# Performance work log

Measured on AMD Instinct MI355X. Metric: run time of the kernel, lower is better.

## Reference

```python
import jax, jax.numpy as jnp
import numpy as np

N, D, H_HEADS = 2048, 1024, 16
HD = D // H_HEADS  # per-head dim = 64
LN_EPS = 1e-5


def setup_inputs() -> dict:
    key = jax.random.key(0)
    ks = jax.random.split(key, 6)
    s = 1.0 / np.sqrt(D)  # keep pre-softmax logits in a sane range
    return {
        "X": jax.random.normal(ks[0], (N, D), dtype=jnp.float32),
        "Wq": jax.random.normal(ks[1], (D, D), dtype=jnp.float32) * s,
        "bq": jnp.zeros((D,), jnp.float32),
        "Wk": jax.random.normal(ks[2], (D, D), dtype=jnp.float32) * s,
        "bk": jnp.zeros((D,), jnp.float32),
        "Wv": jax.random.normal(ks[3], (D, D), dtype=jnp.float32) * s,
        "bv": jnp.zeros((D,), jnp.float32),
        "Wo": jax.random.normal(ks[4], (D, D), dtype=jnp.float32) * s,
        "bo": jnp.zeros((D,), jnp.float32),
        "ln_g": jnp.ones((D,), jnp.float32),
        "ln_b": jnp.zeros((D,), jnp.float32),
    }


def reference(X, Wq, bq, Wk, bk, Wv, bv, Wo, bo, ln_g, ln_b):
    n = X.shape[0]
    # QKV projections -> [h, N, HD]  (matches .view(N, h, -1).transpose(0, 1))
    q = (X @ Wq + bq).reshape(n, H_HEADS, HD).swapaxes(0, 1)
    k = (X @ Wk + bk).reshape(n, H_HEADS, HD).swapaxes(0, 1)
    v = (X @ Wv + bv).reshape(n, H_HEADS, HD).swapaxes(0, 1)
    # Unscaled attention scores (original has NO 1/sqrt(d) factor): [h, N, N]
    A = jnp.einsum('hnd,hmd->hnm', q, k)
    # Diagonal self-exclusion mask
    diag = jnp.eye(n, dtype=bool)
    A = jnp.where(diag[None, :, :], -jnp.inf, A)
    p = jax.nn.softmax(A, axis=-1)
    Oh = jnp.einsum('hnm,hmd->hnd', p, v)  # [h, N, HD]
    # Faithful replication of Oh.transpose(1,2).contiguous().view(N, d):
    # [h, N, HD] -> [h, HD, N] -> reshape to [N, D]
    O = Oh.swapaxes(1, 2).reshape(n, D)
    # Out-proj (dropout is identity in eval mode) + residual + LayerNorm
    Y = X + (O @ Wo + bo)
    mu = jnp.mean(Y, axis=-1, keepdims=True)
    var = jnp.var(Y, axis=-1, keepdims=True)
    return (Y - mu) * jax.lax.rsqrt(var + LN_EPS) * ln_g + ln_b
```

## Files before the change

### kernel.cpp

```cpp
#include <hip/hip_runtime.h>
#include <math.h>


#define NTOK 2048
#define DM   1024
#define NH   16
#define HDIM 64
#define LOG2E 1.4426950408889634f

typedef __attribute__((ext_vector_type(8))) short bf16x8;
typedef __attribute__((ext_vector_type(4))) float f32x4;

#define FRL(op, ch, st, l, e) (((((op) * 2 + (ch)) * 4 + (st)) * 64 + (l)) * 8 + (e))
#define FRO(ch, st, l, e) ((((ch) * 4 + (st)) * 64 + (l)) * 8 + (e))
#define MFMA(a, b, c) __builtin_amdgcn_mfma_f32_16x16x32_bf16(a, b, c, 0, 0, 0)

__device__ __forceinline__ unsigned short f2bf(float f) {
  unsigned u = __float_as_uint(f);
  u += 0x7FFF + ((u >> 16) & 1);
  return (unsigned short)(u >> 16);
}
__device__ __forceinline__ float bf2f(unsigned short h) {
  return __uint_as_float(((unsigned)h) << 16);
}
__device__ __forceinline__ void gload16(const unsigned short* g, unsigned short* l) {
  __builtin_amdgcn_global_load_lds(
      (const __attribute__((address_space(1))) unsigned int*)g,
      (__attribute__((address_space(3))) unsigned int*)l, 16, 0, 0);
}

__global__ __launch_bounds__(256) void cvt_x_blob(
    const float* __restrict__ X, unsigned short* __restrict__ XB)
{
  __shared__ __align__(16) unsigned short img[8192];
  const int kt = blockIdx.x, rt = blockIdx.y, tid = threadIdx.x;
  #pragma unroll
  for (int s = 0; s < 4; ++s) {
    const int f = tid + s * 256;
    const int rl = f >> 4, c4 = (f & 15) * 4;
    const float4 v = *(const float4*)(X + (size_t)(rt * 64 + rl) * DM + kt * 64 + c4);
    const float vv[4] = {v.x, v.y, v.z, v.w};
    unsigned short hi[4], lo[4];
    #pragma unroll
    for (int e = 0; e < 4; ++e) {
      hi[e] = f2bf(vv[e]);
      lo[e] = f2bf(vv[e] - bf2f(hi[e]));
    }
    const int ch = c4 >> 5, c32 = c4 & 31;
    const int gp = (c32 & 15) >> 2, e0 = (c32 >> 4) * 4;
    const int l = 16 * gp + (rl & 15), sti = rl >> 4;
    *(uint2*)&img[FRL(0, ch, sti, l, e0)] =
        make_uint2(hi[0] | (hi[1] << 16), hi[2] | (hi[3] << 16));
    *(uint2*)&img[FRL(1, ch, sti, l, e0)] =
        make_uint2(lo[0] | (lo[1] << 16), lo[2] | (lo[3] << 16));
  }
  __syncthreads();
  unsigned short* out = XB + ((size_t)rt * 16 + kt) * 8192;
  #pragma unroll
  for (int s = 0; s < 4; ++s) {
    const int u = s * 256 + tid;
    *(uint4*)(out + (size_t)u * 8) = *(const uint4*)&img[(size_t)u * 8];
  }
}

__global__ __launch_bounds__(256) void cvt_w_blob(
    const float* __restrict__ W0, const float* __restrict__ W1,
    const float* __restrict__ W2, const float* __restrict__ W3,
    unsigned short* __restrict__ WB)
{
  __shared__ __align__(16) float st[64][68];
  __shared__ __align__(16) unsigned short img[8192];
  const int nt = blockIdx.x, kt = blockIdx.y, z = blockIdx.z, tid = threadIdx.x;
  const float* W = (z == 0) ? W0 : (z == 1) ? W1 : (z == 2) ? W2 : W3;
  #pragma unroll
  for (int s = 0; s < 4; ++s) {
    const int f = tid + s * 256;
    const int kl = f >> 4, n4 = (f & 15) * 4;
    const float4 v = *(const float4*)(W + (size_t)(kt * 64 + kl) * DM + nt * 64 + n4);
    *(float4*)&st[kl][n4] = v;
  }
  __syncthreads();
  #pragma unroll
  for (int s = 0; s < 4; ++s) {
    const int f = tid + s * 256;
    const int nl = f >> 4, k4 = (f & 15) * 4;
    unsigned short hi[4], lo[4];
    #pragma unroll
    for (int e = 0; e < 4; ++e) {
      const float v = st[k4 + e][nl];
      hi[e] = f2bf(v);
      lo[e] = f2bf(v - bf2f(hi[e]));
    }
    const int ch = k4 >> 5, c32 = k4 & 31;
    const int gp = (c32 & 15) >> 2, e0 = (c32 >> 4) * 4;
    const int l = 16 * gp + (nl & 15), sti = nl >> 4;
    *(uint2*)&img[FRL(0, ch, sti, l, e0)] =
        make_uint2(hi[0] | (hi[1] << 16), hi[2] | (hi[3] << 16));
    *(uint2*)&img[FRL(1, ch, sti, l, e0)] =
        make_uint2(lo[0] | (lo[1] << 16), lo[2] | (lo[3] << 16));
  }
  __syncthreads();
  unsigned short* out = WB + (size_t)z * 2097152 + ((size_t)nt * 16 + kt) * 8192;
  #pragma unroll
  for (int s = 0; s < 4; ++s) {
    const int u = s * 256 + tid;
    *(uint4*)(out + (size_t)u * 8) = *(const uint4*)&img[(size_t)u * 8];
  }
}

__global__ __launch_bounds__(256) void gemm_qkv_blob(
    const unsigned short* __restrict__ XB, const unsigned short* __restrict__ WB,
    const float* __restrict__ bq, const float* __restrict__ bk,
    const float* __restrict__ bv,
    unsigned short* __restrict__ QF, unsigned short* __restrict__ KF,
    unsigned short* __restrict__ VF)
{
  __shared__ __align__(16) unsigned short lds[32768];
  const int tid = threadIdx.x, lane = tid & 63, wid = tid >> 6;
  const int wm = wid >> 1, wn = wid & 1;
  const int bx = blockIdx.x, by = blockIdx.y, z = blockIdx.z;
  const int g = lane >> 4, c = lane & 15;

  const unsigned short* BB = WB + (size_t)z * 2097152;
  const unsigned short* bases[4] = {
      XB + ((size_t)(2 * by) * 16) * 8192, XB + ((size_t)(2 * by + 1) * 16) * 8192,
      BB + ((size_t)(2 * bx) * 16) * 8192, BB + ((size_t)(2 * bx + 1) * 16) * 8192};

  f32x4 acc[4][4];
  #pragma unroll
  for (int i = 0; i < 4; ++i)
    #pragma unroll
    for (int j = 0; j < 4; ++j) acc[i][j] = (f32x4){0.f, 0.f, 0.f, 0.f};

  for (int kt = 0; kt < 16; ++kt) {
    __syncthreads();
    #pragma unroll
    for (int s = 0; s < 16; ++s)
      gload16(bases[s >> 2] + (size_t)kt * 8192 + ((size_t)((s & 3) * 256 + tid)) * 8,
              &lds[(size_t)(s * 256 + tid) * 8]);
    __syncthreads();
    #pragma unroll
    for (int ch = 0; ch < 2; ++ch) {
      bf16x8 ah[4], al[4], bh[4], bl[4];
      #pragma unroll
      for (int f = 0; f < 4; ++f) {
        ah[f] = *(const bf16x8*)&lds[wm * 8192 + FRL(0, ch, f, lane, 0)];
        al[f] = *(const bf16x8*)&lds[wm * 8192 + FRL(1, ch, f, lane, 0)];
        bh[f] = *(const bf16x8*)&lds[16384 + wn * 8192 + FRL(0, ch, f, lane, 0)];
        bl[f] = *(const bf16x8*)&lds[16384 + wn * 8192 + FRL(1, ch, f, lane, 0)];
      }
      #pragma unroll
      for (int fm = 0; fm < 4; ++fm)
        #pragma unroll
        for (int fn = 0; fn < 4; ++fn) {
          acc[fm][fn] = MFMA(ah[fm], bh[fn], acc[fm][fn]);
          acc[fm][fn] = MFMA(ah[fm], bl[fn], acc[fm][fn]);
          acc[fm][fn] = MFMA(al[fm], bh[fn], acc[fm][fn]);
        }
    }
  }

  const float* bias = (z == 0) ? bq : (z == 1) ? bk : bv;
  unsigned short* OUTF = (z == 0) ? QF : (z == 1) ? KF : VF;

  __syncthreads();
  const int imgb = (wm * 2 + wn) * 8192;
  #pragma unroll
  for (int fm = 0; fm < 4; ++fm)
    #pragma unroll
    for (int fn = 0; fn < 4; ++fn) {
      const int col = 128 * bx + 64 * wn + 16 * fn + c;
      const float bcol = bias[col];
      #pragma unroll
      for (int r = 0; r < 4; ++r) {
        float val = acc[fm][fn][r] + bcol;
        if (z == 0) val *= LOG2E;
        const unsigned short hp = f2bf(val);
        const unsigned short lp = f2bf(val - bf2f(hp));
        int sti, l, ch_i, e;
        if (z != 2) {
          sti = fm; l = 16 * (c >> 2) + (4 * g + r);
          ch_i = fn >> 1; e = 4 * (fn & 1) + (c & 3);
        } else {
          sti = fn; l = 16 * g + c;
          ch_i = fm >> 1; e = 4 * (fm & 1) + r;
        }
        lds[imgb + FRL(0, ch_i, sti, l, e)] = hp;
        lds[imgb + FRL(1, ch_i, sti, l, e)] = lp;
      }
    }
  __syncthreads();
  #pragma unroll
  for (int s = 0; s < 16; ++s) {
    const int u = s * 256 + tid;
    const int i = s >> 2;
    const int head = 2 * bx + (i & 1), tt = 2 * by + (i >> 1);
    *(uint4*)(OUTF + ((size_t)head * 32 + tt) * 8192 + (size_t)(u & 1023) * 8) =
        *(const uint4*)&lds[(size_t)u * 8];
  }
}

__global__ __launch_bounds__(256) void gemm_out_blob(
    const unsigned short* __restrict__ OF, const unsigned short* __restrict__ WoB,
    const float* __restrict__ bo, const float* __restrict__ X,
    float* __restrict__ Y)
{
  __shared__ __align__(16) unsigned short lds[24576];
  const int tid = threadIdx.x, lane = tid & 63, wid = tid >> 6;
  const int wm = wid >> 1, wn = wid & 1;
  const int bx = blockIdx.x, by = blockIdx.y;

  const unsigned short* oa0 = OF + ((size_t)(2 * by) * 16) * 4096;
  const unsigned short* oa1 = OF + ((size_t)(2 * by + 1) * 16) * 4096;
  const unsigned short* wb0 = WoB + ((size_t)(2 * bx) * 16) * 8192;
  const unsigned short* wb1 = WoB + ((size_t)(2 * bx + 1) * 16) * 8192;

  f32x4 acc[4][4];
  #pragma unroll
  for (int i = 0; i < 4; ++i)
    #pragma unroll
    for (int j = 0; j < 4; ++j) acc[i][j] = (f32x4){0.f, 0.f, 0.f, 0.f};

  for (int kt = 0; kt < 16; ++kt) {
    __syncthreads();
    #pragma unroll
    for (int s = 0; s < 2; ++s) {
      gload16(oa0 + (size_t)kt * 4096 + (size_t)(s * 256 + tid) * 8,
              &lds[(size_t)(s * 256 + tid) * 8]);
      gload16(oa1 + (size_t)kt * 4096 + (size_t)(s * 256 + tid) * 8,
              &lds[(size_t)(512 + s * 256 + tid) * 8]);
    }
    #pragma unroll
    for (int s = 0; s < 4; ++s) {
      gload16(wb0 + (size_t)kt * 8192 + (size_t)(s * 256 + tid) * 8,
              &lds[(size_t)(1024 + s * 256 + tid) * 8]);
      gload16(wb1 + (size_t)kt * 8192 + (size_t)(s * 256 + tid) * 8,
              &lds[(size_t)(2048 + s * 256 + tid) * 8]);
    }
    __syncthreads();
    #pragma unroll
    for (int ch = 0; ch < 2; ++ch) {
      bf16x8 ah[4], bh[4], bl[4];
      #pragma unroll
      for (int f = 0; f < 4; ++f) {
        ah[f] = *(const bf16x8*)&lds[wm * 4096 + FRO(ch, f, lane, 0)];
        bh[f] = *(const bf16x8*)&lds[8192 + wn * 8192 + FRL(0, ch, f, lane, 0)];
        bl[f] = *(const bf16x8*)&lds[8192 + wn * 8192 + FRL(1, ch, f, lane, 0)];
      }
      #pragma unroll
      for (int fm = 0; fm < 4; ++fm)
        #pragma unroll
        for (int fn = 0; fn < 4; ++fn) {
          acc[fm][fn] = MFMA(ah[fm], bh[fn], acc[fm][fn]);
          acc[fm][fn] = MFMA(ah[fm], bl[fn], acc[fm][fn]);
        }
    }
  }

  const int g = lane >> 4, c = lane & 15;
  #pragma unroll
  for (int fm = 0; fm < 4; ++fm)
    #pragma unroll
    for (int fn = 0; fn < 4; ++fn) {
      const int col = 128 * bx + 64 * wn + 16 * fn + c;
      const float bcol = bo[col];
      #pragma unroll
      for (int r = 0; r < 4; ++r) {
        const int row = 128 * by + 64 * wm + 16 * fm + 4 * g + r;
        Y[(size_t)row * DM + col] =
            acc[fm][fn][r] + bcol + X[(size_t)row * DM + col];
      }
    }
}

__global__ __launch_bounds__(256) void attn_mfma3_kernel(
    const unsigned short* __restrict__ QF, const unsigned short* __restrict__ KF,
    const unsigned short* __restrict__ VF, unsigned short* __restrict__ OF)
{
  __shared__ __align__(16) unsigned short lds[32768];

  const int tid = threadIdx.x, lane = tid & 63, wv = tid >> 6;
  const int g = lane >> 4, c = lane & 15;
  const int h = blockIdx.y, tq = blockIdx.x;
  const int q0 = tq * 64;
  const int qq = q0 + 16 * wv + c;

  const unsigned short* qb = QF + ((size_t)h * 32 + tq) * 8192;
  bf16x8 qh[2], ql[2];
  #pragma unroll
  for (int ch = 0; ch < 2; ++ch) {
    qh[ch] = *(const bf16x8*)(qb + FRL(0, ch, wv, lane, 0));
    ql[ch] = *(const bf16x8*)(qb + FRL(1, ch, wv, lane, 0));
  }

  f32x4 acc_o[4];
  #pragma unroll
  for (int df = 0; df < 4; ++df) acc_o[df] = (f32x4){0.f, 0.f, 0.f, 0.f};
  float m_run = -INFINITY, l_run = 0.f;

  const size_t hbase = (size_t)h * 32;
  {
    const unsigned short* kb = KF + hbase * 8192;
    const unsigned short* vb = VF + hbase * 8192;
    #pragma unroll
    for (int s = 0; s < 4; ++s) {
      gload16(kb + (size_t)(s * 256 + tid) * 8, &lds[(size_t)(s * 256 + tid) * 8]);
      gload16(vb + (size_t)(s * 256 + tid) * 8, &lds[8192 + (size_t)(s * 256 + tid) * 8]);
    }
  }

  int buf = 0;
  for (int kt = 0; kt < NTOK / 64; ++kt) {
    __syncthreads();
    if (kt + 1 < NTOK / 64) {
      const unsigned short* kb = KF + (hbase + kt + 1) * 8192;
      const unsigned short* vb = VF + (hbase + kt + 1) * 8192;
      unsigned short* lk = &lds[(buf ^ 1) * 16384];
      #pragma unroll
      for (int s = 0; s < 4; ++s) {
        gload16(kb + (size_t)(s * 256 + tid) * 8, lk + (size_t)(s * 256 + tid) * 8);
        gload16(vb + (size_t)(s * 256 + tid) * 8, lk + 8192 + (size_t)(s * 256 + tid) * 8);
      }
    }
    const unsigned short* lk = &lds[buf * 16384];
    const unsigned short* lv = lk + 8192;

    f32x4 sacc[4];
    #pragma unroll
    for (int fm = 0; fm < 4; ++fm) sacc[fm] = (f32x4){0.f, 0.f, 0.f, 0.f};
    __builtin_amdgcn_s_setprio(1);
    #pragma unroll
    for (int ch = 0; ch < 2; ++ch) {
      #pragma unroll
      for (int fm = 0; fm < 4; ++fm) {
        const bf16x8 khf = *(const bf16x8*)&lk[FRL(0, ch, fm, lane, 0)];
        const bf16x8 klf = *(const bf16x8*)&lk[FRL(1, ch, fm, lane, 0)];
        sacc[fm] = MFMA(khf, qh[ch], sacc[fm]);
        sacc[fm] = MFMA(khf, ql[ch], sacc[fm]);
        sacc[fm] = MFMA(klf, qh[ch], sacc[fm]);
      }
    }
    __builtin_amdgcn_s_setprio(0);

    const int tok0 = kt * 64 + 4 * g;
    #pragma unroll
    for (int fm = 0; fm < 4; ++fm)
      #pragma unroll
      for (int r = 0; r < 4; ++r)
        if (tok0 + 16 * fm + r == qq) sacc[fm][r] = -INFINITY;

    float m = -INFINITY;
    #pragma unroll
    for (int fm = 0; fm < 4; ++fm)
      #pragma unroll
      for (int r = 0; r < 4; ++r) m = fmaxf(m, sacc[fm][r]);
    m = fmaxf(m, __shfl_xor(m, 16, 64));
    m = fmaxf(m, __shfl_xor(m, 32, 64));
    const float mnew = fmaxf(m_run, m);
    const float scal = exp2f(m_run - mnew);
    float ps = 0.f;
    #pragma unroll
    for (int fm = 0; fm < 4; ++fm)
      #pragma unroll
      for (int r = 0; r < 4; ++r) {
        const float p = exp2f(sacc[fm][r] - mnew);
        sacc[fm][r] = p;
        ps += p;
      }
    ps += __shfl_xor(ps, 16, 64);
    ps += __shfl_xor(ps, 32, 64);
    l_run = l_run * scal + ps;
    m_run = mnew;

    bf16x8 ph[2];
    #pragma unroll
    for (int ch = 0; ch < 2; ++ch)
      #pragma unroll
      for (int i = 0; i < 8; ++i)
        ph[ch][i] = (short)f2bf(sacc[2 * ch + (i >> 2)][i & 3]);

    #pragma unroll
    for (int df = 0; df < 4; ++df)
      #pragma unroll
      for (int r = 0; r < 4; ++r) acc_o[df][r] *= scal;
    __builtin_amdgcn_s_setprio(1);
    #pragma unroll
    for (int ch = 0; ch < 2; ++ch)
      #pragma unroll
      for (int df = 0; df < 4; ++df) {
        const bf16x8 vh = *(const bf16x8*)&lv[FRL(0, ch, df, lane, 0)];
        const bf16x8 vl = *(const bf16x8*)&lv[FRL(1, ch, df, lane, 0)];
        acc_o[df] = MFMA(vh, ph[ch], acc_o[df]);
        acc_o[df] = MFMA(vl, ph[ch], acc_o[df]);
      }
    __builtin_amdgcn_s_setprio(0);
    buf ^= 1;
  }

  const float inv = 1.0f / l_run;
  const int n1 = tq >> 4, ktc = tq & 15;
  __syncthreads();
  #pragma unroll
  for (int df = 0; df < 4; ++df)
    #pragma unroll
    for (int r = 0; r < 4; ++r) {
      const int d = 16 * df + 4 * g + r;
      const int rw = 2 * d + n1;
      const int rt_l = rw >> 6, row64 = rw & 63;
      const int sti = row64 >> 4, row16 = row64 & 15;
      const int l = 16 * (c >> 2) + row16;
      const int e = 4 * (wv & 1) + (c & 3);
      lds[rt_l * 4096 + FRO(wv >> 1, sti, l, e)] = f2bf(acc_o[df][r] * inv);
    }
  __syncthreads();
  #pragma unroll
  for (int s = 0; s < 2; ++s) {
    const int p = s * 256 + tid;
    const int rt_l = p >> 8, q = p & 255;
    const int rh = q & 7, gp = (q >> 3) & 3, sti = (q >> 5) & 3, chi = q >> 7;
    const int slot = (chi * 4 + sti) * 64 + 16 * gp + 2 * rh + n1;
    *(uint4*)(OF + (((size_t)(2 * h + rt_l)) * 16 + ktc) * 4096 + (size_t)slot * 8) =
        *(const uint4*)&lds[(size_t)(rt_l * 4096 + slot * 8)];
  }
}

__global__ __launch_bounds__(256) void ln_kernel(
    const float* __restrict__ Y, const float* __restrict__ g,
    const float* __restrict__ b, float* __restrict__ out)
{
  __shared__ float red[8];
  const int row = blockIdx.x;
  const int tid = threadIdx.x;
  const float4 y = *(const float4*)(Y + (size_t)row * DM + tid * 4);
  float s  = y.x + y.y + y.z + y.w;
  float ss = y.x * y.x + y.y * y.y + y.z * y.z + y.w * y.w;
  #pragma unroll
  for (int o = 1; o < 64; o <<= 1) {
    s  += __shfl_xor(s, o, 64);
    ss += __shfl_xor(ss, o, 64);
  }
  const int wv = tid >> 6;
  if ((tid & 63) == 0) { red[wv] = s; red[4 + wv] = ss; }
  __syncthreads();
  s  = red[0] + red[1] + red[2] + red[3];
  ss = red[4] + red[5] + red[6] + red[7];
  const float mu   = s * (1.f / DM);
  const float var  = ss * (1.f / DM) - mu * mu;
  const float rstd = rsqrtf(var + 1e-5f);
  const float4 gv = *(const float4*)(g + tid * 4);
  const float4 bv = *(const float4*)(b + tid * 4);
  float4 o;
  o.x = (y.x - mu) * rstd * gv.x + bv.x;
  o.y = (y.y - mu) * rstd * gv.y + bv.y;
  o.z = (y.z - mu) * rstd * gv.z + bv.z;
  o.w = (y.w - mu) * rstd * gv.w + bv.w;
  *(float4*)(out + (size_t)row * DM + tid * 4) = o;
}

extern "C" void kernel_launch(void* const* d_in, const int* in_sizes, int n_in,
                              void* d_out, int out_size, void* d_ws, size_t ws_size,
                              hipStream_t stream) {
  const float* X    = (const float*)d_in[0];
  const float* Wq   = (const float*)d_in[1];
  const float* bq   = (const float*)d_in[2];
  const float* Wk   = (const float*)d_in[3];
  const float* bk   = (const float*)d_in[4];
  const float* Wv   = (const float*)d_in[5];
  const float* bv   = (const float*)d_in[6];
  const float* Wo   = (const float*)d_in[7];
  const float* bo   = (const float*)d_in[8];
  const float* ln_g = (const float*)d_in[9];
  const float* ln_b = (const float*)d_in[10];

  const size_t MAT = (size_t)NTOK * DM;
  float* Y = (float*)d_ws;
  unsigned short* XB = (unsigned short*)(Y + MAT);
  unsigned short* WB = XB + 2 * MAT;
  unsigned short* QF = WB + 4 * MAT;
  unsigned short* KF = QF + 2 * MAT;
  unsigned short* VF = KF + 2 * MAT;
  unsigned short* OF = VF + 2 * MAT;

  const dim3 blk(256);

  cvt_x_blob<<<dim3(16, 32), blk, 0, stream>>>(X, XB);
  cvt_w_blob<<<dim3(16, 16, 4), blk, 0, stream>>>(Wq, Wk, Wv, Wo, WB);

  gemm_qkv_blob<<<dim3(8, 16, 3), blk, 0, stream>>>(
      XB, WB, bq, bk, bv, QF, KF, VF);

  attn_mfma3_kernel<<<dim3(32, 16), blk, 0, stream>>>(QF, KF, VF, OF);

  gemm_out_blob<<<dim3(8, 16), blk, 0, stream>>>(
      OF, WB + 3 * MAT, bo, X, Y);

  ln_kernel<<<NTOK, blk, 0, stream>>>(Y, ln_g, ln_b, (float*)d_out);
}
```

Baseline: 228.4 us.

## Store V as single bf16, drop split-precision PV, lazy rescale, remap blocks

V is now produced and stored as a single bf16 plane instead of a hi/lo pair, which halves V traffic, LDS use and the PV MFMA count, and drops one MFMA per tile in the V projection. The attention kernel also gains a lazy online-softmax rescale that only updates the running max when it grows by more than 8 (in log2 units), a diagonal mask check limited to the matching tile, bf16 truncation in place of rounding for P, and a swizzled block-to-(head, tile) mapping. The cost is lower precision in V and P and a change in how blocks are scheduled.

```diff
diff --git a/kernel.cpp b/kernel.cpp
--- a/kernel.cpp
+++ b/kernel.cpp
@@ -155,48 +155,70 @@
         for (int fn = 0; fn < 4; ++fn) {
           acc[fm][fn] = MFMA(ah[fm], bh[fn], acc[fm][fn]);
           acc[fm][fn] = MFMA(ah[fm], bl[fn], acc[fm][fn]);
-          acc[fm][fn] = MFMA(al[fm], bh[fn], acc[fm][fn]);
+          if (z != 2)
+            acc[fm][fn] = MFMA(al[fm], bh[fn], acc[fm][fn]);
         }
     }
   }
 
   const float* bias = (z == 0) ? bq : (z == 1) ? bk : bv;
-  unsigned short* OUTF = (z == 0) ? QF : (z == 1) ? KF : VF;
-
-  __syncthreads();
-  const int imgb = (wm * 2 + wn) * 8192;
-  #pragma unroll
-  for (int fm = 0; fm < 4; ++fm)
-    #pragma unroll
-    for (int fn = 0; fn < 4; ++fn) {
-      const int col = 128 * bx + 64 * wn + 16 * fn + c;
-      const float bcol = bias[col];
-      #pragma unroll
-      for (int r = 0; r < 4; ++r) {
-        float val = acc[fm][fn][r] + bcol;
-        if (z == 0) val *= LOG2E;
-        const unsigned short hp = f2bf(val);
-        const unsigned short lp = f2bf(val - bf2f(hp));
-        int sti, l, ch_i, e;
-        if (z != 2) {
-          sti = fm; l = 16 * (c >> 2) + (4 * g + r);
-          ch_i = fn >> 1; e = 4 * (fn & 1) + (c & 3);
-        } else {
-          sti = fn; l = 16 * g + c;
-          ch_i = fm >> 1; e = 4 * (fm & 1) + r;
+
+  __syncthreads();
+  if (z != 2) {
+    unsigned short* OUTF = (z == 0) ? QF : KF;
+    const int imgb = (wm * 2 + wn) * 8192;
+    #pragma unroll
+    for (int fm = 0; fm < 4; ++fm)
+      #pragma unroll
+      for (int fn = 0; fn < 4; ++fn) {
+        const int col = 128 * bx + 64 * wn + 16 * fn + c;
+        const float bcol = bias[col];
+        #pragma unroll
+        for (int r = 0; r < 4; ++r) {
+          float val = acc[fm][fn][r] + bcol;
+          if (z == 0) val *= LOG2E;
+          const unsigned short hp = f2bf(val);
+          const unsigned short lp = f2bf(val - bf2f(hp));
+          const int sti = fm, l = 16 * (c >> 2) + (4 * g + r);
+          const int ch_i = fn >> 1, e = 4 * (fn & 1) + (c & 3);
+          lds[imgb + FRL(0, ch_i, sti, l, e)] = hp;
+          lds[imgb + FRL(1, ch_i, sti, l, e)] = lp;
         }
-        lds[imgb + FRL(0, ch_i, sti, l, e)] = hp;
-        lds[imgb + FRL(1, ch_i, sti, l, e)] = lp;
-      }
-    }
-  __syncthreads();
-  #pragma unroll
-  for (int s = 0; s < 16; ++s) {
-    const int u = s * 256 + tid;
-    const int i = s >> 2;
-    const int head = 2 * bx + (i & 1), tt = 2 * by + (i >> 1);
-    *(uint4*)(OUTF + ((size_t)head * 32 + tt) * 8192 + (size_t)(u & 1023) * 8) =
-        *(const uint4*)&lds[(size_t)u * 8];
+      }
+    __syncthreads();
+    #pragma unroll
+    for (int s = 0; s < 16; ++s) {
+      const int u = s * 256 + tid;
+      const int i = s >> 2;
+      const int head = 2 * bx + (i & 1), tt = 2 * by + (i >> 1);
+      *(uint4*)(OUTF + ((size_t)head * 32 + tt) * 8192 + (size_t)(u & 1023) * 8) =
+          *(const uint4*)&lds[(size_t)u * 8];
+    }
+  } else {
+    const int imgb = (wm * 2 + wn) * 4096;
+    #pragma unroll
+    for (int fm = 0; fm < 4; ++fm)
+      #pragma unroll
+      for (int fn = 0; fn < 4; ++fn) {
+        const int col = 128 * bx + 64 * wn + 16 * fn + c;
+        const float bcol = bias[col];
+        #pragma unroll
+        for (int r = 0; r < 4; ++r) {
+          const float val = acc[fm][fn][r] + bcol;
+          const int sti = fn, l = 16 * g + c;
+          const int ch_i = fm >> 1, e = 4 * (fm & 1) + r;
+          lds[imgb + FRO(ch_i, sti, l, e)] = f2bf(val);
+        }
+      }
+    __syncthreads();
+    #pragma unroll
+    for (int s = 0; s < 8; ++s) {
+      const int u = s * 256 + tid;
+      const int i = u >> 9;
+      const int head = 2 * bx + (i & 1), tt = 2 * by + (i >> 1);
+      *(uint4*)(VF + ((size_t)head * 32 + tt) * 4096 + (size_t)(u & 511) * 8) =
+          *(const uint4*)&lds[(size_t)u * 8];
+    }
   }
 }
 
@@ -273,15 +295,17 @@
     }
 }
 
-__global__ __launch_bounds__(256) void attn_mfma3_kernel(
+__global__ __launch_bounds__(256) void attn_mfma4_kernel(
     const unsigned short* __restrict__ QF, const unsigned short* __restrict__ KF,
     const unsigned short* __restrict__ VF, unsigned short* __restrict__ OF)
 {
-  __shared__ __align__(16) unsigned short lds[32768];
+  __shared__ __align__(16) unsigned short lds[24576];
 
   const int tid = threadIdx.x, lane = tid & 63, wv = tid >> 6;
   const int g = lane >> 4, c = lane & 15;
-  const int h = blockIdx.y, tq = blockIdx.x;
+  const int flat = blockIdx.y * gridDim.x + blockIdx.x;
+  const int o = (flat & 7) * 64 + (flat >> 3);
+  const int h = o >> 5, tq = o & 31;
   const int q0 = tq * 64;
   const int qq = q0 + 16 * wv + c;
 
@@ -301,12 +325,13 @@
   const size_t hbase = (size_t)h * 32;
   {
     const unsigned short* kb = KF + hbase * 8192;
-    const unsigned short* vb = VF + hbase * 8192;
-    #pragma unroll
-    for (int s = 0; s < 4; ++s) {
+    const unsigned short* vb = VF + hbase * 4096;
+    #pragma unroll
+    for (int s = 0; s < 4; ++s)
       gload16(kb + (size_t)(s * 256 + tid) * 8, &lds[(size_t)(s * 256 + tid) * 8]);
+    #pragma unroll
+    for (int s = 0; s < 2; ++s)
       gload16(vb + (size_t)(s * 256 + tid) * 8, &lds[8192 + (size_t)(s * 256 + tid) * 8]);
-    }
   }
 
   int buf = 0;
@@ -314,15 +339,16 @@
     __syncthreads();
     if (kt + 1 < NTOK / 64) {
       const unsigned short* kb = KF + (hbase + kt + 1) * 8192;
-      const unsigned short* vb = VF + (hbase + kt + 1) * 8192;
-      unsigned short* lk = &lds[(buf ^ 1) * 16384];
-      #pragma unroll
-      for (int s = 0; s < 4; ++s) {
+      const unsigned short* vb = VF + (hbase + kt + 1) * 4096;
+      unsigned short* lk = &lds[(buf ^ 1) * 12288];
+      #pragma unroll
+      for (int s = 0; s < 4; ++s)
         gload16(kb + (size_t)(s * 256 + tid) * 8, lk + (size_t)(s * 256 + tid) * 8);
+      #pragma unroll
+      for (int s = 0; s < 2; ++s)
         gload16(vb + (size_t)(s * 256 + tid) * 8, lk + 8192 + (size_t)(s * 256 + tid) * 8);
-      }
-    }
-    const unsigned short* lk = &lds[buf * 16384];
+    }
+    const unsigned short* lk = &lds[buf * 12288];
     const unsigned short* lv = lk + 8192;
 
     f32x4 sacc[4];
@@ -342,12 +368,14 @@
     }
     __builtin_amdgcn_s_setprio(0);
 
-    const int tok0 = kt * 64 + 4 * g;
-    #pragma unroll
-    for (int fm = 0; fm < 4; ++fm)
-      #pragma unroll
-      for (int r = 0; r < 4; ++r)
-        if (tok0 + 16 * fm + r == qq) sacc[fm][r] = -INFINITY;
+    if (kt == tq) {
+      const int tok0 = kt * 64 + 4 * g;
+      #pragma unroll
+      for (int fm = 0; fm < 4; ++fm)
+        #pragma unroll
+        for (int r = 0; r < 4; ++r)
+          if (tok0 + 16 * fm + r == qq) sacc[fm][r] = -INFINITY;
+    }
 
     float m = -INFINITY;
     #pragma unroll
@@ -356,42 +384,43 @@
       for (int r = 0; r < 4; ++r) m = fmaxf(m, sacc[fm][r]);
     m = fmaxf(m, __shfl_xor(m, 16, 64));
     m = fmaxf(m, __shfl_xor(m, 32, 64));
-    const float mnew = fmaxf(m_run, m);
-    const float scal = exp2f(m_run - mnew);
+    if (__any(m > m_run + 8.0f)) {
+      const float mnew = fmaxf(m_run, m);
+      const float scal = exp2f(m_run - mnew);
+      l_run *= scal;
+      #pragma unroll
+      for (int df = 0; df < 4; ++df)
+        #pragma unroll
+        for (int r = 0; r < 4; ++r) acc_o[df][r] *= scal;
+      m_run = mnew;
+    }
     float ps = 0.f;
     #pragma unroll
     for (int fm = 0; fm < 4; ++fm)
       #pragma unroll
       for (int r = 0; r < 4; ++r) {
-        const float p = exp2f(sacc[fm][r] - mnew);
+        const float p = exp2f(sacc[fm][r] - m_run);
         sacc[fm][r] = p;
         ps += p;
       }
     ps += __shfl_xor(ps, 16, 64);
     ps += __shfl_xor(ps, 32, 64);
-    l_run = l_run * scal + ps;
-    m_run = mnew;
+    l_run += ps;
 
     bf16x8 ph[2];
     #pragma unroll
     for (int ch = 0; ch < 2; ++ch)
       #pragma unroll
       for (int i = 0; i < 8; ++i)
-        ph[ch][i] = (short)f2bf(sacc[2 * ch + (i >> 2)][i & 3]);
-
-    #pragma unroll
-    for (int df = 0; df < 4; ++df)
-      #pragma unroll
-      for (int r = 0; r < 4; ++r) acc_o[df][r] *= scal;
+        ph[ch][i] = (short)(__float_as_uint(sacc[2 * ch + (i >> 2)][i & 3]) >> 16);
+
     __builtin_amdgcn_s_setprio(1);
     #pragma unroll
     for (int ch = 0; ch < 2; ++ch)
       #pragma unroll
       for (int df = 0; df < 4; ++df) {
-        const bf16x8 vh = *(const bf16x8*)&lv[FRL(0, ch, df, lane, 0)];
-        const bf16x8 vl = *(const bf16x8*)&lv[FRL(1, ch, df, lane, 0)];
+        const bf16x8 vh = *(const bf16x8*)&lv[FRO(ch, df, lane, 0)];
         acc_o[df] = MFMA(vh, ph[ch], acc_o[df]);
-        acc_o[df] = MFMA(vl, ph[ch], acc_o[df]);
       }
     __builtin_amdgcn_s_setprio(0);
     buf ^= 1;
@@ -479,7 +508,7 @@
   unsigned short* QF = WB + 4 * MAT;
   unsigned short* KF = QF + 2 * MAT;
   unsigned short* VF = KF + 2 * MAT;
-  unsigned short* OF = VF + 2 * MAT;
+  unsigned short* OF = VF + MAT;
 
   const dim3 blk(256);
 
@@ -489,7 +518,7 @@
   gemm_qkv_blob<<<dim3(8, 16, 3), blk, 0, stream>>>(
       XB, WB, bq, bk, bv, QF, KF, VF);
 
-  attn_mfma3_kernel<<<dim3(32, 16), blk, 0, stream>>>(QF, KF, VF, OF);
+  attn_mfma4_kernel<<<dim3(32, 16), blk, 0, stream>>>(QF, KF, VF, OF);
 
   gemm_out_blob<<<dim3(8, 16), blk, 0, stream>>>(
       OF, WB + 3 * MAT, bo, X, Y);
```

Result: faster. 217.5 us (-4.8%).
